# Kernel optimization log

Hardware: AMD Instinct MI355X
Metric: run time of the kernel (lower is better)

The kernel has to match this reference:

```python
import jax, jax.numpy as jnp
import numpy as np


def setup_inputs() -> dict:
    key = jax.random.key(0)
    k1, k2, k3, k4 = jax.random.split(key, 4)
    B, L1, L2, H, A = 64, 512, 512, 1024, 1024
    reps_lt = jax.random.normal(k1, (B, L1, H), dtype=jnp.float32)
    reps_rt = jax.random.normal(k2, (B, L2, H), dtype=jnp.float32)
    mask_lt = jnp.ones((B, L1), dtype=jnp.float32)
    mask_rt = jnp.ones((B, L2), dtype=jnp.float32)
    # Keras 'uniform' initializer ~ U(-0.05, 0.05); scale similarly
    attn_w1 = jax.random.uniform(k3, (H, A), dtype=jnp.float32, minval=-0.05, maxval=0.05)
    diagonal_W = jax.random.uniform(k4, (1, 1, A), dtype=jnp.float32, minval=-0.05, maxval=0.05)
    return {
        "reps_lt": reps_lt,
        "reps_rt": reps_rt,
        "mask_lt": mask_lt,
        "mask_rt": mask_rt,
        "attn_w1": attn_w1,
        "diagonal_W": diagonal_W,
    }


def reference(reps_lt, reps_rt, mask_lt, mask_rt, attn_w1, diagonal_W):
    # Projections: the original does expand_dims + broadcast multiply + sum,
    # which is mathematically a matmul over the hidden dim.
    # attn_w2 aliases attn_w1 because hidden dims are equal.
    attn_lt = jnp.tanh(jnp.einsum('blh,ha->bla', reps_lt, attn_w1))  # [B,L1,A]
    attn_rt = jnp.tanh(jnp.einsum('brh,ha->bra', reps_rt, attn_w1))  # [B,L2,A]
    attn_lt = attn_lt * diagonal_W                                   # diagonal bilinear scale
    # batch_dot([B,L1,A], [B,A,L2]) -> [B,L1,L2]
    attn_value = jnp.einsum('bla,bra->blr', attn_lt, attn_rt)
    # mask (multiplicative, as in original) before softmax
    attn_value = attn_value * mask_lt[:, :, None] * mask_rt[:, None, :]
    attn_prob = jax.nn.softmax(attn_value, axis=-1)
    # mask again after softmax
    attn_prob = attn_prob * mask_lt[:, :, None] * mask_rt[:, None, :]
    return attn_prob
```

## Files before the change

### kernel.cpp

```cpp
#include <hip/hip_runtime.h>
#include <hip/hip_bf16.h>

#define B_ 64
#define L_ 512
#define H_ 1024
#define A_ 1024

typedef short bf16x8 __attribute__((ext_vector_type(8)));
typedef float f32x4 __attribute__((ext_vector_type(4)));

__device__ __forceinline__ void gld16(const void* g, void* l) {
  __builtin_amdgcn_global_load_lds((const __attribute__((address_space(1))) void*)g,
                                   (__attribute__((address_space(3))) void*)l, 16, 0, 0);
}

__device__ __forceinline__ unsigned short f2bf(float f) {
  unsigned u = __builtin_bit_cast(unsigned, f);
  u = (u + 0x7fffu + ((u >> 16) & 1u)) >> 16;
  return (unsigned short)u;
}

__device__ __forceinline__ unsigned short cvtbf(float f) {
  __hip_bfloat16 b = __float2bfloat16(f);
  return __builtin_bit_cast(unsigned short, b);
}

__device__ __forceinline__ float fast_tanh(float x) {
  float e = __expf(2.f * x);
  float r = __builtin_amdgcn_rcpf(e + 1.f);
  return __builtin_fmaf(-2.f, r, 1.f);
}

__global__ __launch_bounds__(256) void cvt_kernel(const float* __restrict__ lt,
                                                  const float* __restrict__ rt,
                                                  unsigned short* __restrict__ xb) {
  const size_t NC = (size_t)B_ * L_ * H_ / 8;
  size_t stride = (size_t)gridDim.x * blockDim.x;
  for (size_t c = (size_t)blockIdx.x * blockDim.x + threadIdx.x; c < 2 * NC; c += stride) {
    const float* src = (c < NC) ? (lt + c * 8) : (rt + (c - NC) * 8);
    float4 v0 = ((const float4*)src)[0];
    float4 v1 = ((const float4*)src)[1];
    bf16x8 o;
    o[0] = (short)cvtbf(v0.x); o[1] = (short)cvtbf(v0.y);
    o[2] = (short)cvtbf(v0.z); o[3] = (short)cvtbf(v0.w);
    o[4] = (short)cvtbf(v1.x); o[5] = (short)cvtbf(v1.y);
    o[6] = (short)cvtbf(v1.z); o[7] = (short)cvtbf(v1.w);
    *(bf16x8*)(xb + c * 8) = o;
  }
}

__global__ __launch_bounds__(256) void wtrans_kernel(const float* __restrict__ W,
                                                     unsigned short* __restrict__ Wt) {
  __shared__ float tile[32][33];
  int tx = threadIdx.x & 31, ty = threadIdx.x >> 5;
  int a0 = (blockIdx.x & 31) << 5, h0 = (blockIdx.x >> 5) << 5;
#pragma unroll
  for (int i = 0; i < 4; ++i) {
    int h = ty + i * 8;
    tile[h][tx] = W[(size_t)(h0 + h) * A_ + a0 + tx];
  }
  __syncthreads();
#pragma unroll
  for (int i = 0; i < 4; ++i) {
    int a = ty + i * 8;
    Wt[(size_t)(a0 + a) * H_ + h0 + tx] = f2bf(tile[tx][a]);
  }
}

#define STG_A(buf, h, kt) {                                                 \
    gld16(gA##h    + (kt) * 64, &As[buf][(h) * 8192 + lofs]);               \
    gld16(gA##h##b + (kt) * 64, &As[buf][(h) * 8192 + 4096 + lofs]); }
#define STG_B(buf, h, kt) {                                                 \
    gld16(gB##h    + (kt) * 64, &Bs[buf][(h) * 8192 + lofs]);               \
    gld16(gB##h##b + (kt) * 64, &Bs[buf][(h) * 8192 + 4096 + lofs]); }

#define LOAD_BQ(buf) { _Pragma("unroll") for (int ni = 0; ni < 4; ++ni) {   \
    int brow = wc * 64 + ni * 16 + l15;                                     \
    bq[ni][0] = *(const bf16x8*)&Bs[buf][brow * 64 + rd0];                  \
    bq[ni][1] = *(const bf16x8*)&Bs[buf][brow * 64 + rd1]; } }

#define PHASE(q, buf, STAGE_OP, CKPT) {                                     \
    bf16x8 aq0, aq1, aq2, aq3;                                              \
    { int ar = wr * 128 + (q) * 32 + l15;                                   \
      aq0 = *(const bf16x8*)&As[buf][ar * 64 + rd0];                        \
      aq1 = *(const bf16x8*)&As[buf][ar * 64 + rd1];                        \
      aq2 = *(const bf16x8*)&As[buf][(ar + 16) * 64 + rd0];                 \
      aq3 = *(const bf16x8*)&As[buf][(ar + 16) * 64 + rd1]; }               \
    STAGE_OP;                                                               \
    asm volatile("s_barrier" ::: "memory");                                 \
    __builtin_amdgcn_s_setprio(1);                                          \
    _Pragma("unroll") for (int ni = 0; ni < 4; ++ni) {                      \
      acc[(q)*2][ni] = __builtin_amdgcn_mfma_f32_16x16x32_bf16(             \
          aq0, bq[ni][0], acc[(q)*2][ni], 0, 0, 0);                         \
      acc[(q)*2][ni] = __builtin_amdgcn_mfma_f32_16x16x32_bf16(             \
          aq1, bq[ni][1], acc[(q)*2][ni], 0, 0, 0);                         \
      acc[(q)*2+1][ni] = __builtin_amdgcn_mfma_f32_16x16x32_bf16(           \
          aq2, bq[ni][0], acc[(q)*2+1][ni], 0, 0, 0);                       \
      acc[(q)*2+1][ni] = __builtin_amdgcn_mfma_f32_16x16x32_bf16(           \
          aq3, bq[ni][1], acc[(q)*2+1][ni], 0, 0, 0); }                     \
    __builtin_amdgcn_s_setprio(0);                                          \
    if (CKPT) asm volatile("s_waitcnt vmcnt(4)" ::: "memory");              \
    asm volatile("s_barrier" ::: "memory"); }

#define CONV_ITER(kt1, kt2, kt3) {                                          \
    LOAD_BQ(0);                                                             \
    PHASE(0, 0, STG_A(1, 0, kt1), 0);                                       \
    PHASE(1, 0, STG_A(1, 1, kt1), 0);                                       \
    PHASE(2, 0, STG_B(0, 0, kt2), 0);                                       \
    PHASE(3, 0, STG_B(0, 1, kt2), 1);                                       \
    LOAD_BQ(1);                                                             \
    PHASE(0, 1, STG_A(0, 0, kt2), 0);                                       \
    PHASE(1, 1, STG_A(0, 1, kt2), 0);                                       \
    PHASE(2, 1, STG_B(1, 0, kt3), 0);                                       \
    PHASE(3, 1, STG_B(1, 1, kt3), 1); }

#define CONVEYOR_LIT()                                                      \
  STG_B(0, 0, 0); STG_B(0, 1, 0);                                           \
  STG_A(0, 0, 0); STG_A(0, 1, 0);                                           \
  STG_B(1, 0, 1); STG_B(1, 1, 1);                                           \
  asm volatile("s_waitcnt vmcnt(4)" ::: "memory");                          \
  asm volatile("s_barrier" ::: "memory");                                   \
  CONV_ITER(1, 2, 3)   CONV_ITER(3, 4, 5)   CONV_ITER(5, 6, 7)              \
  CONV_ITER(7, 8, 9)   CONV_ITER(9, 10, 11) CONV_ITER(11, 12, 13)           \
  CONV_ITER(13, 14, 15) CONV_ITER(15, 0, 1)

__global__ __launch_bounds__(512, 2) void proj8_kernel(
    const unsigned short* __restrict__ Xb, const unsigned short* __restrict__ Wt,
    const float* __restrict__ diag, unsigned short* __restrict__ Pb) {
  __shared__ unsigned short As[2][256 * 64];
  __shared__ unsigned short Bs[2][256 * 64];
  int t = threadIdx.x;
  int lane = t & 63, wave = t >> 6;
  int wr = wave >> 2, wc = wave & 3;
  int l15 = lane & 15, l4 = lane >> 4;

  int bid = (int)blockIdx.x;
  int x = bid & 7, k = bid >> 3;
  int mt = x + 8 * (k >> 2);
  int nt = k & 3;
  int mrow0 = mt << 8, ncol0 = nt << 8;
  int isLt = (mt < 128);

  int rs = t >> 3, ss = t & 7;
  const unsigned short* gA0 = Xb + (size_t)(mrow0 + rs) * H_ + ((ss ^ (rs & 7)) << 3);
  const unsigned short* gA0b = gA0 + (size_t)64 * H_;
  const unsigned short* gA1  = gA0 + (size_t)128 * H_;
  const unsigned short* gA1b = gA0 + (size_t)192 * H_;
  const unsigned short* gB0 = Wt + (size_t)(ncol0 + rs) * H_ + ((ss ^ (rs & 7)) << 3);
  const unsigned short* gB0b = gB0 + (size_t)64 * H_;
  const unsigned short* gB1  = gB0 + (size_t)128 * H_;
  const unsigned short* gB1b = gB0 + (size_t)192 * H_;
  int lofs = (rs * 8 + ss) * 8;

  int rd0 = (l4 ^ (l15 & 7)) * 8;
  int rd1 = ((4 + l4) ^ (l15 & 7)) * 8;

  f32x4 acc[8][4] = {};
  bf16x8 bq[4][2];

  CONVEYOR_LIT();

#pragma unroll
  for (int mi = 0; mi < 8; ++mi) {
#pragma unroll
    for (int ni = 0; ni < 4; ++ni) {
      int col = ncol0 + wc * 64 + ni * 16 + l15;
      float d = isLt ? diag[col] : 1.0f;
#pragma unroll
      for (int rr = 0; rr < 4; ++rr) {
        int row = mrow0 + wr * 128 + mi * 16 + l4 * 4 + rr;
        Pb[(size_t)row * A_ + col] = f2bf(fast_tanh(acc[mi][ni][rr]) * d);
      }
    }
  }
}

__global__ __launch_bounds__(512, 2) void score8_kernel(
    const unsigned short* __restrict__ Pb,
    const float* __restrict__ mask_lt, const float* __restrict__ mask_rt,
    float* __restrict__ out) {
  __shared__ unsigned short As[2][256 * 64];
  __shared__ unsigned short Bs[2][256 * 64];
  int t = threadIdx.x;
  int lane = t & 63, wave = t >> 6;
  int wr = wave >> 2, wc = wave & 3;
  int l15 = lane & 15, l4 = lane >> 4;

  int bid = (int)blockIdx.x;
  int x = bid & 7, k = bid >> 3;
  int pm = x + 8 * (k >> 1);
  int b = pm >> 1, mt = pm & 1, nt = k & 1;

  int arow0 = b * 512 + mt * 256;
  int brow0 = 32768 + b * 512 + nt * 256;

  int rs = t >> 3, ss = t & 7;
  const unsigned short* gA0 = Pb + (size_t)(arow0 + rs) * H_ + ((ss ^ (rs & 7)) << 3);
  const unsigned short* gA0b = gA0 + (size_t)64 * H_;
  const unsigned short* gA1  = gA0 + (size_t)128 * H_;
  const unsigned short* gA1b = gA0 + (size_t)192 * H_;
  const unsigned short* gB0 = Pb + (size_t)(brow0 + rs) * H_ + ((ss ^ (rs & 7)) << 3);
  const unsigned short* gB0b = gB0 + (size_t)64 * H_;
  const unsigned short* gB1  = gB0 + (size_t)128 * H_;
  const unsigned short* gB1b = gB0 + (size_t)192 * H_;
  int lofs = (rs * 8 + ss) * 8;

  int rd0 = (l4 ^ (l15 & 7)) * 8;
  int rd1 = ((4 + l4) ^ (l15 & 7)) * 8;

  f32x4 acc[8][4] = {};
  bf16x8 bq[4][2];

  CONVEYOR_LIT();

  const float* mlp = mask_lt + b * L_;
  const float* mrp = mask_rt + b * L_;
  float* obase = out + (size_t)b * L_ * L_;
#pragma unroll
  for (int mi = 0; mi < 8; ++mi) {
#pragma unroll
    for (int ni = 0; ni < 4; ++ni) {
      int col = nt * 256 + wc * 64 + ni * 16 + l15;
      float mr = mrp[col];
#pragma unroll
      for (int rr = 0; rr < 4; ++rr) {
        int row = mt * 256 + wr * 128 + mi * 16 + l4 * 4 + rr;
        obase[(size_t)row * L_ + col] = acc[mi][ni][rr] * mlp[row] * mr;
      }
    }
  }
}

__global__ __launch_bounds__(256) void softmax_kernel(float* __restrict__ out,
                                                      const float* __restrict__ mask_lt,
                                                      const float* __restrict__ mask_rt) {
  int lane = threadIdx.x & 63, wave = threadIdx.x >> 6;
  int row = (int)blockIdx.x * 4 + wave;
  int b = row >> 9;
  float* p = out + (size_t)row * L_;
  float4 v0 = *(const float4*)(p + lane * 8);
  float4 v1 = *(const float4*)(p + lane * 8 + 4);
  float m = fmaxf(fmaxf(fmaxf(v0.x, v0.y), fmaxf(v0.z, v0.w)),
                  fmaxf(fmaxf(v1.x, v1.y), fmaxf(v1.z, v1.w)));
#pragma unroll
  for (int off = 32; off; off >>= 1) m = fmaxf(m, __shfl_xor(m, off));
  float e0 = __expf(v0.x - m), e1 = __expf(v0.y - m), e2 = __expf(v0.z - m), e3 = __expf(v0.w - m);
  float e4 = __expf(v1.x - m), e5 = __expf(v1.y - m), e6 = __expf(v1.z - m), e7 = __expf(v1.w - m);
  float s = ((e0 + e1) + (e2 + e3)) + ((e4 + e5) + (e6 + e7));
#pragma unroll
  for (int off = 32; off; off >>= 1) s += __shfl_xor(s, off);
  float sc = (1.0f / s) * mask_lt[row];
  const float* mrp = mask_rt + (b << 9) + lane * 8;
  float4 mr0 = *(const float4*)mrp;
  float4 mr1 = *(const float4*)(mrp + 4);
  float4 o0 = make_float4(e0 * sc * mr0.x, e1 * sc * mr0.y, e2 * sc * mr0.z, e3 * sc * mr0.w);
  float4 o1 = make_float4(e4 * sc * mr1.x, e5 * sc * mr1.y, e6 * sc * mr1.z, e7 * sc * mr1.w);
  *(float4*)(p + lane * 8) = o0;
  *(float4*)(p + lane * 8 + 4) = o1;
}

extern "C" void kernel_launch(void* const* d_in, const int* in_sizes, int n_in,
                              void* d_out, int out_size, void* d_ws, size_t ws_size,
                              hipStream_t stream) {
  const float* reps_lt = (const float*)d_in[0];
  const float* reps_rt = (const float*)d_in[1];
  const float* mask_lt = (const float*)d_in[2];
  const float* mask_rt = (const float*)d_in[3];
  const float* attn_w1 = (const float*)d_in[4];
  const float* diag    = (const float*)d_in[5];
  float* out = (float*)d_out;

  unsigned short* wt = (unsigned short*)d_ws;
  unsigned short* pb = wt + (size_t)H_ * A_;
  unsigned short* xb = pb + (size_t)B_ * L_ * A_ * 2;

  hipLaunchKernelGGL(wtrans_kernel, dim3(1024), dim3(256), 0, stream, attn_w1, wt);
  hipLaunchKernelGGL(cvt_kernel, dim3(8192), dim3(256), 0, stream,
                     reps_lt, reps_rt, xb);
  hipLaunchKernelGGL(proj8_kernel, dim3(1024), dim3(512), 0, stream,
                     xb, wt, diag, pb);
  hipLaunchKernelGGL(score8_kernel, dim3(256), dim3(512), 0, stream,
                     pb, mask_lt, mask_rt, out);
  hipLaunchKernelGGL(softmax_kernel, dim3(8192), dim3(256), 0, stream,
                     out, mask_lt, mask_rt);
}
```

Baseline: 295.4 us.

## Make projection kernel persistent over N tiles and drop wasted tail prefetch

The projection kernel now launches one block per 256-row M tile and loops over the four 256-column N tiles inside the block, instead of one block per (M,N) tile. The next N tile's prologue loads are issued before the epilogue stores of the current tile, so those loads overlap the tanh/store work. The final conveyor iteration also stops prefetching nonexistent K tiles and drains with vmcnt(0). The trade-off is fewer blocks (256 rather than 1024, with 2 per CU possible), which may leave CUs idle or unbalanced, and each block now runs work serially that used to run in parallel across blocks.

```diff
diff --git a/kernel.cpp b/kernel.cpp
--- a/kernel.cpp
+++ b/kernel.cpp
@@ -99,7 +99,8 @@
       acc[(q)*2+1][ni] = __builtin_amdgcn_mfma_f32_16x16x32_bf16(           \
           aq3, bq[ni][1], acc[(q)*2+1][ni], 0, 0, 0); }                     \
     __builtin_amdgcn_s_setprio(0);                                          \
-    if (CKPT) asm volatile("s_waitcnt vmcnt(4)" ::: "memory");              \
+    if ((CKPT) == 1) asm volatile("s_waitcnt vmcnt(4)" ::: "memory");       \
+    if ((CKPT) == 2) asm volatile("s_waitcnt vmcnt(0)" ::: "memory");       \
     asm volatile("s_barrier" ::: "memory"); }
 
 #define CONV_ITER(kt1, kt2, kt3) {                                          \
@@ -114,15 +115,27 @@
     PHASE(2, 1, STG_B(1, 0, kt3), 0);                                       \
     PHASE(3, 1, STG_B(1, 1, kt3), 1); }
 
-#define CONVEYOR_LIT()                                                      \
+#define CONV_ITER_LAST() {                                                  \
+    LOAD_BQ(0);                                                             \
+    PHASE(0, 0, STG_A(1, 0, 15), 0);                                        \
+    PHASE(1, 0, STG_A(1, 1, 15), 0);                                        \
+    PHASE(2, 0, ;, 0);                                                      \
+    PHASE(3, 0, ;, 2);                                                      \
+    LOAD_BQ(1);                                                             \
+    PHASE(0, 1, ;, 0);                                                      \
+    PHASE(1, 1, ;, 0);                                                      \
+    PHASE(2, 1, ;, 0);                                                      \
+    PHASE(3, 1, ;, 0); }
+
+#define CONV_BODY()                                                         \
+  CONV_ITER(1, 2, 3)   CONV_ITER(3, 4, 5)   CONV_ITER(5, 6, 7)              \
+  CONV_ITER(7, 8, 9)   CONV_ITER(9, 10, 11) CONV_ITER(11, 12, 13)           \
+  CONV_ITER(13, 14, 15) CONV_ITER_LAST()
+
+#define PROLOGUE()                                                          \
   STG_B(0, 0, 0); STG_B(0, 1, 0);                                           \
   STG_A(0, 0, 0); STG_A(0, 1, 0);                                           \
-  STG_B(1, 0, 1); STG_B(1, 1, 1);                                           \
-  asm volatile("s_waitcnt vmcnt(4)" ::: "memory");                          \
-  asm volatile("s_barrier" ::: "memory");                                   \
-  CONV_ITER(1, 2, 3)   CONV_ITER(3, 4, 5)   CONV_ITER(5, 6, 7)              \
-  CONV_ITER(7, 8, 9)   CONV_ITER(9, 10, 11) CONV_ITER(11, 12, 13)           \
-  CONV_ITER(13, 14, 15) CONV_ITER(15, 0, 1)
+  STG_B(1, 0, 1); STG_B(1, 1, 1);
 
 __global__ __launch_bounds__(512, 2) void proj8_kernel(
     const unsigned short* __restrict__ Xb, const unsigned short* __restrict__ Wt,
@@ -134,11 +147,8 @@
   int wr = wave >> 2, wc = wave & 3;
   int l15 = lane & 15, l4 = lane >> 4;
 
-  int bid = (int)blockIdx.x;
-  int x = bid & 7, k = bid >> 3;
-  int mt = x + 8 * (k >> 2);
-  int nt = k & 3;
-  int mrow0 = mt << 8, ncol0 = nt << 8;
+  int mt = (int)blockIdx.x;
+  int mrow0 = mt << 8;
   int isLt = (mt < 128);
 
   int rs = t >> 3, ss = t & 7;
@@ -146,7 +156,7 @@
   const unsigned short* gA0b = gA0 + (size_t)64 * H_;
   const unsigned short* gA1  = gA0 + (size_t)128 * H_;
   const unsigned short* gA1b = gA0 + (size_t)192 * H_;
-  const unsigned short* gB0 = Wt + (size_t)(ncol0 + rs) * H_ + ((ss ^ (rs & 7)) << 3);
+  const unsigned short* gB0 = Wt + (size_t)rs * H_ + ((ss ^ (rs & 7)) << 3);
   const unsigned short* gB0b = gB0 + (size_t)64 * H_;
   const unsigned short* gB1  = gB0 + (size_t)128 * H_;
   const unsigned short* gB1b = gB0 + (size_t)192 * H_;
@@ -155,21 +165,41 @@
   int rd0 = (l4 ^ (l15 & 7)) * 8;
   int rd1 = ((4 + l4) ^ (l15 & 7)) * 8;
 
-  f32x4 acc[8][4] = {};
+  f32x4 acc[8][4];
   bf16x8 bq[4][2];
 
-  CONVEYOR_LIT();
-
-#pragma unroll
-  for (int mi = 0; mi < 8; ++mi) {
-#pragma unroll
-    for (int ni = 0; ni < 4; ++ni) {
-      int col = ncol0 + wc * 64 + ni * 16 + l15;
-      float d = isLt ? diag[col] : 1.0f;
-#pragma unroll
-      for (int rr = 0; rr < 4; ++rr) {
-        int row = mrow0 + wr * 128 + mi * 16 + l4 * 4 + rr;
-        Pb[(size_t)row * A_ + col] = f2bf(fast_tanh(acc[mi][ni][rr]) * d);
+  PROLOGUE();
+
+#pragma unroll 1
+  for (int nt = 0; nt < 4; ++nt) {
+#pragma unroll
+    for (int mi = 0; mi < 8; ++mi)
+#pragma unroll
+      for (int ni = 0; ni < 4; ++ni) acc[mi][ni] = f32x4{0.f, 0.f, 0.f, 0.f};
+
+    asm volatile("s_waitcnt vmcnt(4)" ::: "memory");
+    asm volatile("s_barrier" ::: "memory");
+
+    CONV_BODY();
+
+    if (nt < 3) {
+      gB0 += (size_t)256 * H_; gB0b += (size_t)256 * H_;
+      gB1 += (size_t)256 * H_; gB1b += (size_t)256 * H_;
+      PROLOGUE();
+    }
+
+    int ncol0 = nt << 8;
+#pragma unroll
+    for (int mi = 0; mi < 8; ++mi) {
+#pragma unroll
+      for (int ni = 0; ni < 4; ++ni) {
+        int col = ncol0 + wc * 64 + ni * 16 + l15;
+        float d = isLt ? diag[col] : 1.0f;
+#pragma unroll
+        for (int rr = 0; rr < 4; ++rr) {
+          int row = mrow0 + wr * 128 + mi * 16 + l4 * 4 + rr;
+          Pb[(size_t)row * A_ + col] = f2bf(fast_tanh(acc[mi][ni][rr]) * d);
+        }
       }
     }
   }
@@ -211,7 +241,10 @@
   f32x4 acc[8][4] = {};
   bf16x8 bq[4][2];
 
-  CONVEYOR_LIT();
+  PROLOGUE();
+  asm volatile("s_waitcnt vmcnt(4)" ::: "memory");
+  asm volatile("s_barrier" ::: "memory");
+  CONV_BODY();
 
   const float* mlp = mask_lt + b * L_;
   const float* mrp = mask_rt + b * L_;
@@ -277,7 +310,7 @@
   hipLaunchKernelGGL(wtrans_kernel, dim3(1024), dim3(256), 0, stream, attn_w1, wt);
   hipLaunchKernelGGL(cvt_kernel, dim3(8192), dim3(256), 0, stream,
                      reps_lt, reps_rt, xb);
-  hipLaunchKernelGGL(proj8_kernel, dim3(1024), dim3(512), 0, stream,
+  hipLaunchKernelGGL(proj8_kernel, dim3(256), dim3(512), 0, stream,
                      xb, wt, diag, pb);
   hipLaunchKernelGGL(score8_kernel, dim3(256), dim3(512), 0, stream,
                      pb, mask_lt, mask_rt, out);
```

Result: slower. 449.1 us (+52.0%).

## Fuse score GEMM with row softmax using full-row 128x512 tiles

Applied to the files above, without the earlier changes.

Replaces the separate score GEMM and softmax kernels with one kernel in which each block computes a 128-row by full 512-column tile. Row max and sum are reduced in registers and through LDS, so the output is written once already normalized. This removes the extra 64MB read and write of the fp32 score matrix and one kernel launch. In exchange the GEMM tile shape and pipeline change (K step 32, triple buffering, split B loads), the block carries more accumulator registers, and the occupancy hint is dropped.

```diff
diff --git a/kernel.cpp b/kernel.cpp
--- a/kernel.cpp
+++ b/kernel.cpp
@@ -175,88 +175,181 @@
   }
 }
 
-__global__ __launch_bounds__(512, 2) void score8_kernel(
+__global__ __launch_bounds__(512) void ssmax_kernel(
     const unsigned short* __restrict__ Pb,
     const float* __restrict__ mask_lt, const float* __restrict__ mask_rt,
     float* __restrict__ out) {
-  __shared__ unsigned short As[2][256 * 64];
-  __shared__ unsigned short Bs[2][256 * 64];
+  __shared__ unsigned short As2[3][128 * 32];
+  __shared__ unsigned short Bs2[3][512 * 32];
   int t = threadIdx.x;
   int lane = t & 63, wave = t >> 6;
   int wr = wave >> 2, wc = wave & 3;
   int l15 = lane & 15, l4 = lane >> 4;
 
   int bid = (int)blockIdx.x;
-  int x = bid & 7, k = bid >> 3;
-  int pm = x + 8 * (k >> 1);
-  int b = pm >> 1, mt = pm & 1, nt = k & 1;
-
-  int arow0 = b * 512 + mt * 256;
-  int brow0 = 32768 + b * 512 + nt * 256;
-
-  int rs = t >> 3, ss = t & 7;
-  const unsigned short* gA0 = Pb + (size_t)(arow0 + rs) * H_ + ((ss ^ (rs & 7)) << 3);
-  const unsigned short* gA0b = gA0 + (size_t)64 * H_;
-  const unsigned short* gA1  = gA0 + (size_t)128 * H_;
-  const unsigned short* gA1b = gA0 + (size_t)192 * H_;
-  const unsigned short* gB0 = Pb + (size_t)(brow0 + rs) * H_ + ((ss ^ (rs & 7)) << 3);
-  const unsigned short* gB0b = gB0 + (size_t)64 * H_;
-  const unsigned short* gB1  = gB0 + (size_t)128 * H_;
-  const unsigned short* gB1b = gB0 + (size_t)192 * H_;
-  int lofs = (rs * 8 + ss) * 8;
-
-  int rd0 = (l4 ^ (l15 & 7)) * 8;
-  int rd1 = ((4 + l4) ^ (l15 & 7)) * 8;
-
-  f32x4 acc[8][4] = {};
-  bf16x8 bq[4][2];
-
-  CONVEYOR_LIT();
-
-  const float* mlp = mask_lt + b * L_;
-  const float* mrp = mask_rt + b * L_;
-  float* obase = out + (size_t)b * L_ * L_;
-#pragma unroll
-  for (int mi = 0; mi < 8; ++mi) {
-#pragma unroll
-    for (int ni = 0; ni < 4; ++ni) {
-      int col = nt * 256 + wc * 64 + ni * 16 + l15;
-      float mr = mrp[col];
-#pragma unroll
-      for (int rr = 0; rr < 4; ++rr) {
-        int row = mt * 256 + wr * 128 + mi * 16 + l4 * 4 + rr;
-        obase[(size_t)row * L_ + col] = acc[mi][ni][rr] * mlp[row] * mr;
+  int g = (bid & 7) * 32 + (bid >> 3);
+  int b = g >> 2, mt = g & 3;
+
+  int arow0 = b * L_ + mt * 128;
+  int brow0 = B_ * L_ + b * L_;
+
+  int ra = t >> 2, ca = t & 3;
+  const unsigned short* gA = Pb + (size_t)(arow0 + ra) * H_ + ((ca ^ ((ra >> 1) & 3)) << 3);
+  const unsigned short* gBu0; const unsigned short* gBu1;
+  const unsigned short* gBu2; const unsigned short* gBu3;
+  int bd0, bd1, bd2, bd3;
+  {
+    int ci, r, c;
+    ci = t;           r = ci >> 2; c = ci & 3;
+    gBu0 = Pb + (size_t)(brow0 + r) * H_ + ((c ^ ((r >> 1) & 3)) << 3); bd0 = ci * 8;
+    ci = 512 + t;     r = ci >> 2; c = ci & 3;
+    gBu1 = Pb + (size_t)(brow0 + r) * H_ + ((c ^ ((r >> 1) & 3)) << 3); bd1 = ci * 8;
+    ci = 1024 + t;    r = ci >> 2; c = ci & 3;
+    gBu2 = Pb + (size_t)(brow0 + r) * H_ + ((c ^ ((r >> 1) & 3)) << 3); bd2 = ci * 8;
+    ci = 1536 + t;    r = ci >> 2; c = ci & 3;
+    gBu3 = Pb + (size_t)(brow0 + r) * H_ + ((c ^ ((r >> 1) & 3)) << 3); bd3 = ci * 8;
+  }
+  int rd = (l4 ^ ((l15 >> 1) & 3)) * 8;
+
+#define SSTG_B01(buf, kt_) { int ko = (kt_) * 32;                  \
+    gld16(gBu0 + ko, &Bs2[buf][bd0]); gld16(gBu1 + ko, &Bs2[buf][bd1]); }
+#define SSTG_B23A(buf, kt_) { int ko = (kt_) * 32;                 \
+    gld16(gBu2 + ko, &Bs2[buf][bd2]); gld16(gBu3 + ko, &Bs2[buf][bd3]); \
+    gld16(gA + ko, &As2[buf][t * 8]); }
+
+  f32x4 acc[4][8] = {};
+
+  SSTG_B01(0, 0); SSTG_B23A(0, 0);
+  SSTG_B01(1, 1); SSTG_B23A(1, 1);
+  asm volatile("s_waitcnt vmcnt(5)" ::: "memory");
+  asm volatile("s_barrier" ::: "memory");
+
+#pragma unroll 1
+  for (int j = 0; j < 32; ++j) {
+    int buf = j - (j / 3) * 3;
+    int nb = buf + 2; if (nb >= 3) nb -= 3;
+    bool st = (j <= 29);
+    const unsigned short* Ac = As2[buf];
+    const unsigned short* Bc = Bs2[buf];
+
+    bf16x8 aq[4], bq[4];
+#pragma unroll
+    for (int mi = 0; mi < 4; ++mi)
+      aq[mi] = *(const bf16x8*)&Ac[(wr * 64 + mi * 16 + l15) * 32 + rd];
+#pragma unroll
+    for (int ni = 0; ni < 4; ++ni)
+      bq[ni] = *(const bf16x8*)&Bc[(wc * 128 + ni * 16 + l15) * 32 + rd];
+    if (st) SSTG_B01(nb, j + 2);
+    asm volatile("s_barrier" ::: "memory");
+    __builtin_amdgcn_s_setprio(1);
+#pragma unroll
+    for (int mi = 0; mi < 4; ++mi)
+#pragma unroll
+      for (int ni = 0; ni < 4; ++ni)
+        acc[mi][ni] = __builtin_amdgcn_mfma_f32_16x16x32_bf16(aq[mi], bq[ni], acc[mi][ni], 0, 0, 0);
+    __builtin_amdgcn_s_setprio(0);
+    asm volatile("s_barrier" ::: "memory");
+
+#pragma unroll
+    for (int ni = 0; ni < 4; ++ni)
+      bq[ni] = *(const bf16x8*)&Bc[(wc * 128 + 64 + ni * 16 + l15) * 32 + rd];
+    if (st) SSTG_B23A(nb, j + 2);
+    asm volatile("s_barrier" ::: "memory");
+    __builtin_amdgcn_s_setprio(1);
+#pragma unroll
+    for (int mi = 0; mi < 4; ++mi)
+#pragma unroll
+      for (int ni = 0; ni < 4; ++ni)
+        acc[mi][ni + 4] = __builtin_amdgcn_mfma_f32_16x16x32_bf16(aq[mi], bq[ni], acc[mi][ni + 4], 0, 0, 0);
+    __builtin_amdgcn_s_setprio(0);
+    if (j < 30)
+      asm volatile("s_waitcnt vmcnt(5)" ::: "memory");
+    else
+      asm volatile("s_waitcnt vmcnt(0)" ::: "memory");
+    asm volatile("s_barrier" ::: "memory");
+  }
+#undef SSTG_B01
+#undef SSTG_B23A
+
+  float* red = (float*)&As2[0][0];
+  float* red2 = red + 512;
+
+  float ml[4][4];
+#pragma unroll
+  for (int mi = 0; mi < 4; ++mi)
+#pragma unroll
+    for (int rr = 0; rr < 4; ++rr)
+      ml[mi][rr] = mask_lt[b * L_ + mt * 128 + wr * 64 + mi * 16 + l4 * 4 + rr];
+  float mr[8];
+#pragma unroll
+  for (int ni = 0; ni < 8; ++ni)
+    mr[ni] = mask_rt[b * L_ + wc * 128 + ni * 16 + l15];
+
+#pragma unroll
+  for (int mi = 0; mi < 4; ++mi)
+#pragma unroll
+    for (int ni = 0; ni < 8; ++ni)
+#pragma unroll
+      for (int rr = 0; rr < 4; ++rr)
+        acc[mi][ni][rr] *= ml[mi][rr] * mr[ni];
+
+#pragma unroll
+  for (int mi = 0; mi < 4; ++mi)
+#pragma unroll
+    for (int rr = 0; rr < 4; ++rr) {
+      float m = acc[mi][0][rr];
+#pragma unroll
+      for (int ni = 1; ni < 8; ++ni) m = fmaxf(m, acc[mi][ni][rr]);
+      m = fmaxf(m, __shfl_xor(m, 1));
+      m = fmaxf(m, __shfl_xor(m, 2));
+      m = fmaxf(m, __shfl_xor(m, 4));
+      m = fmaxf(m, __shfl_xor(m, 8));
+      if (l15 == 0) red[(wr * 64 + mi * 16 + l4 * 4 + rr) * 4 + wc] = m;
+    }
+  __syncthreads();
+  float mfull[4][4];
+#pragma unroll
+  for (int mi = 0; mi < 4; ++mi)
+#pragma unroll
+    for (int rr = 0; rr < 4; ++rr) {
+      float4 v = *(const float4*)&red[(wr * 64 + mi * 16 + l4 * 4 + rr) * 4];
+      mfull[mi][rr] = fmaxf(fmaxf(v.x, v.y), fmaxf(v.z, v.w));
+    }
+
+#pragma unroll
+  for (int mi = 0; mi < 4; ++mi)
+#pragma unroll
+    for (int rr = 0; rr < 4; ++rr) {
+      float s = 0.f;
+#pragma unroll
+      for (int ni = 0; ni < 8; ++ni) {
+        float e = __expf(acc[mi][ni][rr] - mfull[mi][rr]);
+        acc[mi][ni][rr] = e;
+        s += e;
       }
-    }
-  }
-}
-
-__global__ __launch_bounds__(256) void softmax_kernel(float* __restrict__ out,
-                                                      const float* __restrict__ mask_lt,
-                                                      const float* __restrict__ mask_rt) {
-  int lane = threadIdx.x & 63, wave = threadIdx.x >> 6;
-  int row = (int)blockIdx.x * 4 + wave;
-  int b = row >> 9;
-  float* p = out + (size_t)row * L_;
-  float4 v0 = *(const float4*)(p + lane * 8);
-  float4 v1 = *(const float4*)(p + lane * 8 + 4);
-  float m = fmaxf(fmaxf(fmaxf(v0.x, v0.y), fmaxf(v0.z, v0.w)),
-                  fmaxf(fmaxf(v1.x, v1.y), fmaxf(v1.z, v1.w)));
-#pragma unroll
-  for (int off = 32; off; off >>= 1) m = fmaxf(m, __shfl_xor(m, off));
-  float e0 = __expf(v0.x - m), e1 = __expf(v0.y - m), e2 = __expf(v0.z - m), e3 = __expf(v0.w - m);
-  float e4 = __expf(v1.x - m), e5 = __expf(v1.y - m), e6 = __expf(v1.z - m), e7 = __expf(v1.w - m);
-  float s = ((e0 + e1) + (e2 + e3)) + ((e4 + e5) + (e6 + e7));
-#pragma unroll
-  for (int off = 32; off; off >>= 1) s += __shfl_xor(s, off);
-  float sc = (1.0f / s) * mask_lt[row];
-  const float* mrp = mask_rt + (b << 9) + lane * 8;
-  float4 mr0 = *(const float4*)mrp;
-  float4 mr1 = *(const float4*)(mrp + 4);
-  float4 o0 = make_float4(e0 * sc * mr0.x, e1 * sc * mr0.y, e2 * sc * mr0.z, e3 * sc * mr0.w);
-  float4 o1 = make_float4(e4 * sc * mr1.x, e5 * sc * mr1.y, e6 * sc * mr1.z, e7 * sc * mr1.w);
-  *(float4*)(p + lane * 8) = o0;
-  *(float4*)(p + lane * 8 + 4) = o1;
+      s += __shfl_xor(s, 1);
+      s += __shfl_xor(s, 2);
+      s += __shfl_xor(s, 4);
+      s += __shfl_xor(s, 8);
+      if (l15 == 0) red2[(wr * 64 + mi * 16 + l4 * 4 + rr) * 4 + wc] = s;
+    }
+  __syncthreads();
+
+  float* obase = out + (size_t)b * L_ * L_ + (size_t)(mt * 128) * L_;
+#pragma unroll
+  for (int mi = 0; mi < 4; ++mi)
+#pragma unroll
+    for (int rr = 0; rr < 4; ++rr) {
+      int row = wr * 64 + mi * 16 + l4 * 4 + rr;
+      float4 v = *(const float4*)&red2[row * 4];
+      float inv = 1.0f / (((v.x + v.y) + (v.z + v.w)));
+      float scale = inv * ml[mi][rr];
+#pragma unroll
+      for (int ni = 0; ni < 8; ++ni) {
+        int col = wc * 128 + ni * 16 + l15;
+        obase[(size_t)row * L_ + col] = acc[mi][ni][rr] * scale * mr[ni];
+      }
+    }
 }
 
 extern "C" void kernel_launch(void* const* d_in, const int* in_sizes, int n_in,
@@ -279,8 +372,6 @@
                      reps_lt, reps_rt, xb);
   hipLaunchKernelGGL(proj8_kernel, dim3(1024), dim3(512), 0, stream,
                      xb, wt, diag, pb);
-  hipLaunchKernelGGL(score8_kernel, dim3(256), dim3(512), 0, stream,
+  hipLaunchKernelGGL(ssmax_kernel, dim3(256), dim3(512), 0, stream,
                      pb, mask_lt, mask_rt, out);
-  hipLaunchKernelGGL(softmax_kernel, dim3(8192), dim3(256), 0, stream,
-                     out, mask_lt, mask_rt);
-}
+}
```

Measured after the change: 281.4 us. -4.7%, faster.
